# Optimization experiments

Measured on AMD Instinct MI355X. Metric: run time of the kernel, lower is better.

## Reference

```python
import jax, jax.numpy as jnp
import numpy as np

ALPHA = 0.2  # LeakyReLU negative slope


def setup_inputs() -> dict:
    key = jax.random.key(0)
    k1, k2, k3 = jax.random.split(key, 3)
    B, N, F_in, F_out = 8, 2048, 256, 256
    h = jax.random.normal(k1, (B, N, F_in), dtype=jnp.float32)
    adj = jax.random.randint(k2, (B, N, N), 0, 2, dtype=jnp.int32)
    # xavier_uniform for W [F_in, F_out]
    limit = float(np.sqrt(6.0 / (F_in + F_out)))
    W = jax.random.uniform(k3, (F_in, F_out), dtype=jnp.float32, minval=-limit, maxval=limit)
    return {"h": h, "adj": adj, "W": W}


def reference(h, adj, W):
    # h: [B,N,F_in], W: [F_in,F_out] -> Wh: [B,N,F_out]
    Wh = jnp.einsum('bnf,fo->bno', h, W)
    # (Wh_i + Wh_j).sum(-1) == s[p] + s[q] with s = Wh.sum(-1); avoids [B,N,N,F] tensor
    s = Wh.sum(axis=-1)  # [B,N]
    e = jax.nn.leaky_relu(s[:, :, None] + s[:, None, :], negative_slope=ALPHA)  # [B,N,N]
    e = jnp.where(adj == 0, -jnp.inf, e)
    alpha = jax.nn.softmax(e, axis=-1)  # masked softmax over neighbors
    # dropout is identity in eval mode
    h_prime = jnp.einsum('bpq,bqo->bpo', alpha, Wh)  # [B,N,F_out]
    return h_prime
```

## Files before the change

### kernel.cpp

```cpp
#include <hip/hip_runtime.h>
#include <hip/hip_bf16.h>
#include <stdint.h>

#define LEAKY_ALPHA 0.2f

using f32x4 = __attribute__((ext_vector_type(4))) float;
using u32x2 = __attribute__((ext_vector_type(2))) unsigned int;
using u32x4 = __attribute__((ext_vector_type(4))) unsigned int;
using i32x4 = __attribute__((ext_vector_type(4))) int;
using s16x8 = __attribute__((ext_vector_type(8))) short;

static __device__ __forceinline__ unsigned short f2bf(float x) {
  __hip_bfloat16 b = __float2bfloat16(x);
  return __builtin_bit_cast(unsigned short, b);
}

__global__ __launch_bounds__(256) void gat_prep(
    const float* __restrict__ W, __hip_bfloat16* __restrict__ WT,
    float* __restrict__ wsum)
{
  const int o = blockIdx.x;
  const int t = threadIdx.x;
  WT[o * 256 + t] = __float2bfloat16(W[t * 256 + o]);
  float u = W[o * 256 + t];
#pragma unroll
  for (int off = 1; off < 64; off <<= 1) u += __shfl_xor(u, off, 64);
  __shared__ float red[4];
  if ((t & 63) == 0) red[t >> 6] = u;
  __syncthreads();
  if (t == 0) wsum[o] = red[0] + red[1] + red[2] + red[3];
}

__global__ __launch_bounds__(256) void gat_wh2(
    const float* __restrict__ h, const __hip_bfloat16* __restrict__ WT,
    const float* __restrict__ wsum, __hip_bfloat16* __restrict__ WhT,
    float* __restrict__ s)
{
  const int b = blockIdx.x >> 5;
  const int q0 = (blockIdx.x & 31) * 64;
  const int t = threadIdx.x;
  const int wid = t >> 6, lane = t & 63;

  __shared__ __align__(16) unsigned char Bh[64 * 512];
  __shared__ __align__(16) unsigned char Aw[256 * 128];
  __shared__ __align__(16) float wsl[256];

  wsl[t] = wsum[t];
  __syncthreads();

  {
    const int q = t >> 2;
    const int fs = (t & 3) * 64;
    const float* hrow = h + ((size_t)(b * 2048 + q0 + q)) * 256 + fs;
    float sp = 0.f;
#pragma unroll
    for (int c = 0; c < 8; ++c) {
      const f32x4 a  = *(const f32x4*)&hrow[c * 8];
      const f32x4 bq = *(const f32x4*)&hrow[c * 8 + 4];
      const f32x4 wa = *(const f32x4*)&wsl[fs + c * 8];
      const f32x4 wb = *(const f32x4*)&wsl[fs + c * 8 + 4];
      sp += a[0]*wa[0] + a[1]*wa[1] + a[2]*wa[2] + a[3]*wa[3]
          + bq[0]*wb[0] + bq[1]*wb[1] + bq[2]*wb[2] + bq[3]*wb[3];
      u32x4 pk;
      pk[0] = (unsigned)f2bf(a[0])  | ((unsigned)f2bf(a[1])  << 16);
      pk[1] = (unsigned)f2bf(a[2])  | ((unsigned)f2bf(a[3])  << 16);
      pk[2] = (unsigned)f2bf(bq[0]) | ((unsigned)f2bf(bq[1]) << 16);
      pk[3] = (unsigned)f2bf(bq[2]) | ((unsigned)f2bf(bq[3]) << 16);
      const int boff = q * 512 + ((fs * 2 + c * 16) ^ ((q & 7) << 4));
      *(u32x4*)&Bh[boff] = pk;
    }
    sp += __shfl_xor(sp, 1, 64);
    sp += __shfl_xor(sp, 2, 64);
    if ((t & 3) == 0) s[b * 2048 + q0 + q] = sp;
  }

  f32x4 acc[4][4];
#pragma unroll
  for (int i = 0; i < 4; ++i)
#pragma unroll
    for (int j = 0; j < 4; ++j) acc[i][j] = (f32x4)(0.f);

  for (int it = 0; it < 4; ++it) {
    const int f0 = it * 64;
    __syncthreads();
#pragma unroll
    for (int j = 0; j < 8; ++j) {
      const int o = (t >> 3) + 32 * j;
      const int c = t & 7;
      const u32x4 v = *(const u32x4*)&WT[o * 256 + f0 + c * 8];
      *(u32x4*)&Aw[o * 128 + ((c * 16) ^ ((o & 7) << 4))] = v;
    }
    __syncthreads();
#pragma unroll
    for (int kt = 0; kt < 2; ++kt) {
      const int kb = kt * 64 + ((lane >> 4) << 4);
      s16x8 af[4], bf[4];
#pragma unroll
      for (int qt = 0; qt < 4; ++qt) {
        const int qr = qt * 16 + (lane & 15);
        af[qt] = *(const s16x8*)&Bh[qr * 512 + ((f0 * 2 + kb) ^ ((qr & 7) << 4))];
      }
#pragma unroll
      for (int ot = 0; ot < 4; ++ot) {
        const int orow = wid * 64 + ot * 16 + (lane & 15);
        bf[ot] = *(const s16x8*)&Aw[orow * 128 + (kb ^ ((orow & 7) << 4))];
      }
#pragma unroll
      for (int qt = 0; qt < 4; ++qt)
#pragma unroll
        for (int ot = 0; ot < 4; ++ot)
          acc[qt][ot] = __builtin_amdgcn_mfma_f32_16x16x32_bf16(
              af[qt], bf[ot], acc[qt][ot], 0, 0, 0);
    }
  }

  __hip_bfloat16* __restrict__ WhTb = WhT + (size_t)b * 256 * 2048;
#pragma unroll
  for (int qt = 0; qt < 4; ++qt)
#pragma unroll
    for (int ot = 0; ot < 4; ++ot) {
      const int o = wid * 64 + ot * 16 + (lane & 15);
      const int ql = q0 + qt * 16 + ((lane >> 4) << 2);
      u32x2 pk;
      pk[0] = (unsigned)f2bf(acc[qt][ot][0]) | ((unsigned)f2bf(acc[qt][ot][1]) << 16);
      pk[1] = (unsigned)f2bf(acc[qt][ot][2]) | ((unsigned)f2bf(acc[qt][ot][3]) << 16);
      *(u32x2*)&WhTb[(size_t)o * 2048 + ql] = pk;
    }
}

__global__ __launch_bounds__(512, 4) void gat_attn(
    const int* __restrict__ adj, const float* __restrict__ s,
    const __hip_bfloat16* __restrict__ WhT, float* __restrict__ out)
{
  const int N = 2048;
  const int bid = blockIdx.x;
  const int swz = (bid & 7) * 64 + (bid >> 3);
  const int b = swz >> 6;
  const int p0 = (swz & 63) * 32;
  const int t = threadIdx.x;
  const int wid = t >> 6, lane = t & 63;

  __shared__ __align__(16) unsigned char Bs[2][256 * 128];
  __shared__ __align__(16) unsigned char Wt[2][32 * 128];
  __shared__ __align__(16) float red_sh[8];
  __shared__ __align__(16) float l_sh[32];

  const int ep = t >> 4;
  const int eq4 = (t & 15) * 4;
  const int* __restrict__ adjrow = adj + ((size_t)(b * N + p0 + ep)) * N;
  const float* __restrict__ sB = s + b * N;
  const __hip_bfloat16* __restrict__ WhTb = WhT + (size_t)b * 256 * 2048;

  const int grow = t >> 3;
  const int gchunk = t & 7;
  const size_t gsrc_off = (size_t)grow * 2048 + (size_t)((gchunk ^ (grow & 7)) << 3);
  const int ldst = wid * 1024;

  const int wtoff = ep * 128 + ((eq4 * 2) ^ ((ep & 7) << 4));

#pragma unroll
  for (int c = 0; c < 4; ++c)
    __builtin_amdgcn_global_load_lds(
        (const __attribute__((address_space(1))) unsigned int*)(WhTb + gsrc_off + (size_t)c * 64 * 2048),
        (__attribute__((address_space(3))) unsigned int*)&Bs[0][c * 8192 + ldst],
        16, 0, 0);
  i32x4 aE = *(const i32x4*)&adjrow[eq4];
  f32x4 sE = *(const f32x4*)&sB[eq4];
  i32x4 aO = *(const i32x4*)&adjrow[64 + eq4];
  f32x4 sO = *(const f32x4*)&sB[64 + eq4];

  const f32x4 s4 = *(const f32x4*)&sB[t * 4];
  float bm = fmaxf(fmaxf(s4[0], s4[1]), fmaxf(s4[2], s4[3]));
#pragma unroll
  for (int off = 1; off < 64; off <<= 1) bm = fmaxf(bm, __shfl_xor(bm, off, 64));
  if (lane == 0) red_sh[wid] = bm;
  const float s_p = sB[p0 + ep];
  __syncthreads();
  float smax = red_sh[0];
#pragma unroll
  for (int k = 1; k < 8; ++k) smax = fmaxf(smax, red_sh[k]);
  const float xm = s_p + smax;
  const float m_p = (xm > 0.f) ? xm : (LEAKY_ALPHA * xm);

  f32x4 acc[2][2];
#pragma unroll
  for (int pt = 0; pt < 2; ++pt)
#pragma unroll
    for (int ot = 0; ot < 2; ++ot) acc[pt][ot] = (f32x4)(0.f);
  float lacc = 0.f;

  auto tile = [&](int BI, int QQ, i32x4& AV, f32x4& SV) __attribute__((always_inline)) {
    float wv[4];
#pragma unroll
    for (int i = 0; i < 4; ++i) {
      const float x = s_p + SV[i];
      const float le = (x > 0.f) ? x : (LEAKY_ALPHA * x);
      const float w = __expf(le - m_p);
      wv[i] = (AV[i] != 0) ? w : 0.f;
      lacc += wv[i];
    }
    {
      u32x2 pw;
      pw[0] = (unsigned)f2bf(wv[0]) | ((unsigned)f2bf(wv[1]) << 16);
      pw[1] = (unsigned)f2bf(wv[2]) | ((unsigned)f2bf(wv[3]) << 16);
      *(u32x2*)&Wt[BI][wtoff] = pw;
    }
    {
      const int qr = (QQ + 128 < N) ? (QQ + 128) : (N - 64);
      AV = *(const i32x4*)&adjrow[qr + eq4];
      SV = *(const f32x4*)&sB[qr + eq4];
    }
    asm volatile("s_waitcnt vmcnt(2) lgkmcnt(0)" ::: "memory");
    __builtin_amdgcn_s_barrier();
    __builtin_amdgcn_sched_barrier(0);
    {
      const int qg = (QQ + 64 < N) ? (QQ + 64) : (N - 64);
      const __hip_bfloat16* gs = WhTb + qg + gsrc_off;
#pragma unroll
      for (int c = 0; c < 4; ++c)
        __builtin_amdgcn_global_load_lds(
            (const __attribute__((address_space(1))) unsigned int*)(gs + (size_t)c * 64 * 2048),
            (__attribute__((address_space(3))) unsigned int*)&Bs[BI ^ 1][c * 8192 + ldst],
            16, 0, 0);
    }
    {
      s16x8 afr[2][2], bfr[2][2];
#pragma unroll
      for (int pt = 0; pt < 2; ++pt)
#pragma unroll
        for (int kt = 0; kt < 2; ++kt) {
          const int pa = pt * 16 + (lane & 15);
          const int kb = kt * 64 + ((lane >> 4) << 4);
          afr[pt][kt] = *(const s16x8*)&Wt[BI][pa * 128 + (kb ^ ((pa & 7) << 4))];
        }
#pragma unroll
      for (int ot = 0; ot < 2; ++ot)
#pragma unroll
        for (int kt = 0; kt < 2; ++kt) {
          const int ob = wid * 32 + ot * 16 + (lane & 15);
          const int kb = kt * 64 + ((lane >> 4) << 4);
          bfr[ot][kt] = *(const s16x8*)&Bs[BI][ob * 128 + (kb ^ ((ob & 7) << 4))];
        }
      __builtin_amdgcn_s_setprio(1);
#pragma unroll
      for (int pt = 0; pt < 2; ++pt)
#pragma unroll
        for (int ot = 0; ot < 2; ++ot)
#pragma unroll
          for (int kt = 0; kt < 2; ++kt)
            acc[pt][ot] = __builtin_amdgcn_mfma_f32_16x16x32_bf16(
                afr[pt][kt], bfr[ot][kt], acc[pt][ot], 0, 0, 0);
      __builtin_amdgcn_s_setprio(0);
    }
  };

  for (int q0 = 0; q0 < N; q0 += 128) {
    tile(0, q0, aE, sE);
    tile(1, q0 + 64, aO, sO);
  }

  lacc += __shfl_xor(lacc, 1, 64);
  lacc += __shfl_xor(lacc, 2, 64);
  lacc += __shfl_xor(lacc, 4, 64);
  lacc += __shfl_xor(lacc, 8, 64);
  if ((t & 15) == 0) l_sh[ep] = lacc;
  __syncthreads();

#pragma unroll
  for (int pt = 0; pt < 2; ++pt) {
    const f32x4 lv = *(const f32x4*)&l_sh[pt * 16 + ((lane >> 4) << 2)];
    f32x4 inv;
#pragma unroll
    for (int r = 0; r < 4; ++r) inv[r] = 1.f / lv[r];
#pragma unroll
    for (int ot = 0; ot < 2; ++ot) {
      const int o = wid * 32 + ot * 16 + (lane & 15);
#pragma unroll
      for (int r = 0; r < 4; ++r) {
        const int row = p0 + pt * 16 + ((lane >> 4) << 2) + r;
        out[((size_t)(b * N + row)) * 256 + o] = acc[pt][ot][r] * inv[r];
      }
    }
  }
}

extern "C" void kernel_launch(void* const* d_in, const int* in_sizes, int n_in,
                              void* d_out, int out_size, void* d_ws, size_t ws_size,
                              hipStream_t stream) {
  const float* h = (const float*)d_in[0];
  const int* adj = (const int*)d_in[1];
  const float* W = (const float*)d_in[2];
  float* out = (float*)d_out;

  char* ws = (char*)d_ws;
  __hip_bfloat16* WhT = (__hip_bfloat16*)ws;
  float* s = (float*)(ws + (size_t)8 * 1024 * 1024);
  __hip_bfloat16* WT = (__hip_bfloat16*)(ws + (size_t)8 * 1024 * 1024 + 65536);
  float* wsum = (float*)(ws + (size_t)8 * 1024 * 1024 + 65536 + 131072);

  gat_prep<<<256, 256, 0, stream>>>(W, WT, wsum);
  gat_wh2<<<256, 256, 0, stream>>>(h, WT, wsum, WhT, s);
  gat_attn<<<512, 512, 0, stream>>>(adj, s, WhT, out);
}
```

Baseline: 61.12 us.

## Double attention row tile to 64 rows per block, halving WhT reloads

The attention kernel now handles 64 query rows per block instead of 32, and launches 256 blocks instead of 512. Each staged WhT tile is reused across twice as many rows, which halves the global and LDS traffic for Wh. Warps are split into a 2x4 grid over rows and output columns, each holding 2x4 MFMA accumulators, and the s_setprio hints are removed. In exchange there are fewer blocks on the chip, with launch bounds relaxed to 2 blocks per CU, and more registers are used per thread.

```diff
diff --git a/kernel.cpp b/kernel.cpp
--- a/kernel.cpp
+++ b/kernel.cpp
@@ -128,35 +128,37 @@
     }
 }
 
-__global__ __launch_bounds__(512, 4) void gat_attn(
+__global__ __launch_bounds__(512, 2) void gat_attn(
     const int* __restrict__ adj, const float* __restrict__ s,
     const __hip_bfloat16* __restrict__ WhT, float* __restrict__ out)
 {
   const int N = 2048;
   const int bid = blockIdx.x;
-  const int swz = (bid & 7) * 64 + (bid >> 3);
-  const int b = swz >> 6;
-  const int p0 = (swz & 63) * 32;
+  const int swz = (bid & 7) * 32 + (bid >> 3);
+  const int b = swz >> 5;
+  const int p0 = (swz & 31) * 64;
   const int t = threadIdx.x;
   const int wid = t >> 6, lane = t & 63;
 
   __shared__ __align__(16) unsigned char Bs[2][256 * 128];
-  __shared__ __align__(16) unsigned char Wt[2][32 * 128];
+  __shared__ __align__(16) unsigned char Pt[2][64 * 128];
   __shared__ __align__(16) float red_sh[8];
-  __shared__ __align__(16) float l_sh[32];
-
-  const int ep = t >> 4;
-  const int eq4 = (t & 15) * 4;
-  const int* __restrict__ adjrow = adj + ((size_t)(b * N + p0 + ep)) * N;
+  __shared__ __align__(16) float l_sh[64];
+
+  const int sp_row = t >> 3;
+  const int sq8 = (t & 7) * 8;
+  const int* __restrict__ adjrow = adj + ((size_t)(b * N + p0 + sp_row)) * N;
   const float* __restrict__ sB = s + b * N;
   const __hip_bfloat16* __restrict__ WhTb = WhT + (size_t)b * 256 * 2048;
+  const int ptoff = sp_row * 128 + (((t & 7) ^ (sp_row & 7)) << 4);
 
   const int grow = t >> 3;
   const int gchunk = t & 7;
   const size_t gsrc_off = (size_t)grow * 2048 + (size_t)((gchunk ^ (grow & 7)) << 3);
   const int ldst = wid * 1024;
 
-  const int wtoff = ep * 128 + ((eq4 * 2) ^ ((ep & 7) << 4));
+  const int pg = wid >> 2;
+  const int og = wid & 3;
 
 #pragma unroll
   for (int c = 0; c < 4; ++c)
@@ -164,17 +166,21 @@
         (const __attribute__((address_space(1))) unsigned int*)(WhTb + gsrc_off + (size_t)c * 64 * 2048),
         (__attribute__((address_space(3))) unsigned int*)&Bs[0][c * 8192 + ldst],
         16, 0, 0);
-  i32x4 aE = *(const i32x4*)&adjrow[eq4];
-  f32x4 sE = *(const f32x4*)&sB[eq4];
-  i32x4 aO = *(const i32x4*)&adjrow[64 + eq4];
-  f32x4 sO = *(const f32x4*)&sB[64 + eq4];
+  i32x4 aE0 = *(const i32x4*)&adjrow[sq8];
+  i32x4 aE1 = *(const i32x4*)&adjrow[sq8 + 4];
+  f32x4 sE0 = *(const f32x4*)&sB[sq8];
+  f32x4 sE1 = *(const f32x4*)&sB[sq8 + 4];
+  i32x4 aO0 = *(const i32x4*)&adjrow[64 + sq8];
+  i32x4 aO1 = *(const i32x4*)&adjrow[64 + sq8 + 4];
+  f32x4 sO0 = *(const f32x4*)&sB[64 + sq8];
+  f32x4 sO1 = *(const f32x4*)&sB[64 + sq8 + 4];
 
   const f32x4 s4 = *(const f32x4*)&sB[t * 4];
   float bm = fmaxf(fmaxf(s4[0], s4[1]), fmaxf(s4[2], s4[3]));
 #pragma unroll
   for (int off = 1; off < 64; off <<= 1) bm = fmaxf(bm, __shfl_xor(bm, off, 64));
   if (lane == 0) red_sh[wid] = bm;
-  const float s_p = sB[p0 + ep];
+  const float s_p = sB[p0 + sp_row];
   __syncthreads();
   float smax = red_sh[0];
 #pragma unroll
@@ -182,35 +188,48 @@
   const float xm = s_p + smax;
   const float m_p = (xm > 0.f) ? xm : (LEAKY_ALPHA * xm);
 
-  f32x4 acc[2][2];
+  f32x4 acc[2][4];
 #pragma unroll
   for (int pt = 0; pt < 2; ++pt)
 #pragma unroll
-    for (int ot = 0; ot < 2; ++ot) acc[pt][ot] = (f32x4)(0.f);
+    for (int ot = 0; ot < 4; ++ot) acc[pt][ot] = (f32x4)(0.f);
   float lacc = 0.f;
 
-  auto tile = [&](int BI, int QQ, i32x4& AV, f32x4& SV) __attribute__((always_inline)) {
-    float wv[4];
+  auto phase = [&](int BI, int QQ, i32x4& A0, i32x4& A1, f32x4& S0, f32x4& S1)
+      __attribute__((always_inline)) {
+    float wv[8];
 #pragma unroll
     for (int i = 0; i < 4; ++i) {
-      const float x = s_p + SV[i];
+      const float x = s_p + S0[i];
       const float le = (x > 0.f) ? x : (LEAKY_ALPHA * x);
       const float w = __expf(le - m_p);
-      wv[i] = (AV[i] != 0) ? w : 0.f;
+      wv[i] = (A0[i] != 0) ? w : 0.f;
       lacc += wv[i];
     }
+#pragma unroll
+    for (int i = 0; i < 4; ++i) {
+      const float x = s_p + S1[i];
+      const float le = (x > 0.f) ? x : (LEAKY_ALPHA * x);
+      const float w = __expf(le - m_p);
+      wv[4 + i] = (A1[i] != 0) ? w : 0.f;
+      lacc += wv[4 + i];
+    }
     {
-      u32x2 pw;
-      pw[0] = (unsigned)f2bf(wv[0]) | ((unsigned)f2bf(wv[1]) << 16);
-      pw[1] = (unsigned)f2bf(wv[2]) | ((unsigned)f2bf(wv[3]) << 16);
-      *(u32x2*)&Wt[BI][wtoff] = pw;
+      u32x4 pw;
+#pragma unroll
+      for (int k2 = 0; k2 < 4; ++k2)
+        pw[k2] = (unsigned)f2bf(wv[2 * k2]) |
+                 ((unsigned)f2bf(wv[2 * k2 + 1]) << 16);
+      *(u32x4*)&Pt[BI][ptoff] = pw;
     }
     {
       const int qr = (QQ + 128 < N) ? (QQ + 128) : (N - 64);
-      AV = *(const i32x4*)&adjrow[qr + eq4];
-      SV = *(const f32x4*)&sB[qr + eq4];
-    }
-    asm volatile("s_waitcnt vmcnt(2) lgkmcnt(0)" ::: "memory");
+      A0 = *(const i32x4*)&adjrow[qr + sq8];
+      A1 = *(const i32x4*)&adjrow[qr + sq8 + 4];
+      S0 = *(const f32x4*)&sB[qr + sq8];
+      S1 = *(const f32x4*)&sB[qr + sq8 + 4];
+    }
+    asm volatile("s_waitcnt vmcnt(4) lgkmcnt(0)" ::: "memory");
     __builtin_amdgcn_s_barrier();
     __builtin_amdgcn_sched_barrier(0);
     {
@@ -224,60 +243,58 @@
             16, 0, 0);
     }
     {
-      s16x8 afr[2][2], bfr[2][2];
+      s16x8 afr[2][2], bfr[4][2];
 #pragma unroll
       for (int pt = 0; pt < 2; ++pt)
 #pragma unroll
         for (int kt = 0; kt < 2; ++kt) {
-          const int pa = pt * 16 + (lane & 15);
-          const int kb = kt * 64 + ((lane >> 4) << 4);
-          afr[pt][kt] = *(const s16x8*)&Wt[BI][pa * 128 + (kb ^ ((pa & 7) << 4))];
+          const int pa = pg * 32 + pt * 16 + (lane & 15);
+          const int ck = (kt * 4 + (lane >> 4)) ^ (pa & 7);
+          afr[pt][kt] = *(const s16x8*)&Pt[BI][pa * 128 + ck * 16];
         }
 #pragma unroll
-      for (int ot = 0; ot < 2; ++ot)
+      for (int ot = 0; ot < 4; ++ot)
 #pragma unroll
         for (int kt = 0; kt < 2; ++kt) {
-          const int ob = wid * 32 + ot * 16 + (lane & 15);
-          const int kb = kt * 64 + ((lane >> 4) << 4);
-          bfr[ot][kt] = *(const s16x8*)&Bs[BI][ob * 128 + (kb ^ ((ob & 7) << 4))];
+          const int ob = og * 64 + ot * 16 + (lane & 15);
+          const int ck = (kt * 4 + (lane >> 4)) ^ (ob & 7);
+          bfr[ot][kt] = *(const s16x8*)&Bs[BI][ob * 128 + ck * 16];
         }
-      __builtin_amdgcn_s_setprio(1);
 #pragma unroll
       for (int pt = 0; pt < 2; ++pt)
 #pragma unroll
-        for (int ot = 0; ot < 2; ++ot)
+        for (int ot = 0; ot < 4; ++ot)
 #pragma unroll
           for (int kt = 0; kt < 2; ++kt)
             acc[pt][ot] = __builtin_amdgcn_mfma_f32_16x16x32_bf16(
                 afr[pt][kt], bfr[ot][kt], acc[pt][ot], 0, 0, 0);
-      __builtin_amdgcn_s_setprio(0);
     }
   };
 
   for (int q0 = 0; q0 < N; q0 += 128) {
-    tile(0, q0, aE, sE);
-    tile(1, q0 + 64, aO, sO);
+    phase(0, q0, aE0, aE1, sE0, sE1);
+    phase(1, q0 + 64, aO0, aO1, sO0, sO1);
   }
 
   lacc += __shfl_xor(lacc, 1, 64);
   lacc += __shfl_xor(lacc, 2, 64);
   lacc += __shfl_xor(lacc, 4, 64);
-  lacc += __shfl_xor(lacc, 8, 64);
-  if ((t & 15) == 0) l_sh[ep] = lacc;
+  if ((t & 7) == 0) l_sh[sp_row] = lacc;
   __syncthreads();
 
 #pragma unroll
   for (int pt = 0; pt < 2; ++pt) {
-    const f32x4 lv = *(const f32x4*)&l_sh[pt * 16 + ((lane >> 4) << 2)];
+    const int pb = pg * 32 + pt * 16 + ((lane >> 4) << 2);
+    const f32x4 lv = *(const f32x4*)&l_sh[pb];
     f32x4 inv;
 #pragma unroll
     for (int r = 0; r < 4; ++r) inv[r] = 1.f / lv[r];
 #pragma unroll
-    for (int ot = 0; ot < 2; ++ot) {
-      const int o = wid * 32 + ot * 16 + (lane & 15);
+    for (int ot = 0; ot < 4; ++ot) {
+      const int o = og * 64 + ot * 16 + (lane & 15);
 #pragma unroll
       for (int r = 0; r < 4; ++r) {
-        const int row = p0 + pt * 16 + ((lane >> 4) << 2) + r;
+        const int row = p0 + pb + r;
         out[((size_t)(b * N + row)) * 256 + o] = acc[pt][ot][r] * inv[r];
       }
     }
@@ -300,5 +317,5 @@
 
   gat_prep<<<256, 256, 0, stream>>>(W, WT, wsum);
   gat_wh2<<<256, 256, 0, stream>>>(h, WT, wsum, WhT, s);
-  gat_attn<<<512, 512, 0, stream>>>(adj, s, WhT, out);
-}
+  gat_attn<<<256, 512, 0, stream>>>(adj, s, WhT, out);
+}
```

Result: slower. 63.90 us (+4.6%).
